# Kernel tuning notes

Hardware: AMD Instinct MI355X
Metric: run time of the kernel (lower is better)

Reference implementation:

```python
import jax, jax.numpy as jnp
import numpy as np
from jax import lax

NUM_CHANNELS = 3
NUM_HEADS = 8
PATCH = 16  # projection_dim = 3 * 16 * 16 = 768
EPS = 1e-5


def setup_inputs() -> dict:
    key = jax.random.key(0)
    ks = jax.random.split(key, 16)
    B, N, D, Hdim = 4, 1024, 768, 3072
    H = NUM_HEADS

    def init(k, shape, fan_in):
        bound = 1.0 / np.sqrt(fan_in)
        return jax.random.uniform(k, shape, jnp.float32, -bound, bound)

    return {
        "x": jax.random.normal(ks[0], (B, N, D), jnp.float32),
        # 3x3 conv QKV projections over per-patch [3,16,16] images (no bias, qkv_bias=False)
        "qconv_w": init(ks[1], (NUM_CHANNELS, NUM_CHANNELS, 3, 3), NUM_CHANNELS * 9),
        "kconv_w": init(ks[2], (NUM_CHANNELS, NUM_CHANNELS, 3, 3), NUM_CHANNELS * 9),
        "vconv_w": init(ks[3], (NUM_CHANNELS, NUM_CHANNELS, 3, 3), NUM_CHANNELS * 9),
        # 1x1 conv mixing heads of the attention map + BatchNorm2d(heads)
        "reatten_w": init(ks[4], (H, H), H),
        "reatten_b": init(ks[5], (H,), H),
        "bn_g": jnp.ones((H,), jnp.float32),
        "bn_b": jnp.zeros((H,), jnp.float32),
        # output projection (Linear dim->dim)
        "proj_w": init(ks[6], (D, D), D),
        "proj_b": init(ks[7], (D,), D),
        # LayerNorm over (num_patches, projection_dim) jointly
        "ln_g": jnp.ones((N, D), jnp.float32),
        "ln_b": jnp.zeros((N, D), jnp.float32),
        # FeedForward
        "ff_w1": init(ks[8], (Hdim, D), D),
        "ff_b1": init(ks[9], (Hdim,), D),
        "ff_w2": init(ks[10], (D, Hdim), Hdim),
        "ff_b2": init(ks[11], (D,), Hdim),
    }


def _conv3x3(x, w):
    # x: [BN, C, p, p], w: [C, C, 3, 3], stride 1, SAME padding
    return lax.conv_general_dilated(x, w, (1, 1), "SAME",
                                    dimension_numbers=("NCHW", "OIHW", "NCHW"))


def _layernorm_2d(x, g, b):
    # LayerNorm over last two axes (N, D) jointly, biased variance, eps=1e-5
    mu = jnp.mean(x, axis=(-2, -1), keepdims=True)
    var = jnp.mean(jnp.square(x - mu), axis=(-2, -1), keepdims=True)
    return (x - mu) * lax.rsqrt(var + EPS) * g + b


def _encoder_fwd(x, qconv_w, kconv_w, vconv_w, reatten_w, reatten_b,
                 bn_g, bn_b, proj_w, proj_b, ln_g, ln_b,
                 ff_w1, ff_b1, ff_w2, ff_b2):
    B, N, D = x.shape
    H = NUM_HEADS
    hd = D // H
    scale = hd ** -0.5

    # --- ReAttention ---
    xi = x.reshape(B * N, NUM_CHANNELS, PATCH, PATCH)

    def qkv(w):
        y = _conv3x3(xi, w).reshape(B, N, H, hd)
        return y.transpose(0, 2, 1, 3)  # [B, H, N, hd]

    q, k, v = qkv(qconv_w), qkv(kconv_w), qkv(vconv_w)

    attn = jax.nn.softmax(jnp.einsum("bhnd,bhmd->bhnm", q, k) * scale, axis=-1)

    # learned cross-head 1x1 conv + BatchNorm2d (training-mode batch stats)
    attn = jnp.einsum("gh,bhnm->bgnm", reatten_w, attn) + reatten_b[None, :, None, None]
    mu = jnp.mean(attn, axis=(0, 2, 3), keepdims=True)
    var = jnp.mean(jnp.square(attn - mu), axis=(0, 2, 3), keepdims=True)
    attn = (attn - mu) * lax.rsqrt(var + EPS)
    attn = attn * bn_g[None, :, None, None] + bn_b[None, :, None, None]

    out = jnp.einsum("bhnm,bhmd->bhnd", attn, v)
    out = out.transpose(0, 2, 1, 3).reshape(B, N, D)
    out = out @ proj_w.T + proj_b

    # --- residual + LN ---
    x1 = _layernorm_2d(x + out, ln_g, ln_b)

    # --- FeedForward (exact GELU) + residual + LN ---
    h = jax.nn.gelu(x1 @ ff_w1.T + ff_b1, approximate=False)
    ff = h @ ff_w2.T + ff_b2
    return _layernorm_2d(x1 + ff, ln_g, ln_b)


def reference(x, qconv_w, kconv_w, vconv_w, reatten_w, reatten_b,
              bn_g, bn_b, proj_w, proj_b, ln_g, ln_b,
              ff_w1, ff_b1, ff_w2, ff_b2):
    return _encoder_fwd(x, qconv_w, kconv_w, vconv_w, reatten_w, reatten_b,
                        bn_g, bn_b, proj_w, proj_b, ln_g, ln_b,
                        ff_w1, ff_b1, ff_w2, ff_b2)
```

## Files before the change

kernel.cpp:

```cpp
#include <hip/hip_runtime.h>
#include <math.h>


typedef unsigned short u16;
typedef unsigned int u32;
typedef __bf16 bf16x8 __attribute__((ext_vector_type(8)));
typedef float f32x4 __attribute__((ext_vector_type(4)));

#define EPSV 1e-5f
#define SL2E 0.14724444620253177f
#define EXPC -11.541560327111707f

__device__ __forceinline__ u16 f2bf(float f) {
  union { float f; u32 u; } v; v.f = f;
  u32 u = v.u + 0x7fffu + ((v.u >> 16) & 1u);
  return (u16)(u >> 16);
}
__device__ __forceinline__ float bf2f(u16 h) {
  union { u32 u; float f; } v; v.u = ((u32)h) << 16; return v.f;
}
__device__ __forceinline__ f32x4 mfma16(bf16x8 a, bf16x8 b, f32x4 c) {
  return __builtin_amdgcn_mfma_f32_16x16x32_bf16(a, b, c, 0, 0, 0);
}
__device__ __forceinline__ void gload16(const void* gp, void* lp) {
  __builtin_amdgcn_global_load_lds(
      (const __attribute__((address_space(1))) u32*)gp,
      (__attribute__((address_space(3))) u32*)lp, 16, 0, 0);
}

struct KS { int off[3]; int hl[3]; };
__device__ __forceinline__ KS ks_init(int t) {
  KS ks;
  int lane = t & 63;
  int lh = lane >> 4, l15 = lane & 15;
  #pragma unroll
  for (int j = 0; j < 3; ++j) {
    int G = j * 512 + t;
    int hl = (G >= 768) ? 1 : 0;
    int C = (G - hl * 768) >> 6;
    int chunk = C / 6, r = C - 6 * chunk;
    int kk = r >> 1, c1 = r & 1;
    int m = chunk * 32 + ((l15 >> 2) << 3) + (c1 << 2) + (l15 & 3);
    ks.off[j] = m * 96 + kk * 32 + lh * 8;
    ks.hl[j] = hl;
  }
  return ks;
}
__device__ __forceinline__ void ks_stage(const u16* __restrict__ khi,
    const u16* __restrict__ klo, size_t rowel, const KS& ks, u16* Kb, int t) {
  int w = t >> 6;
  #pragma unroll
  for (int j = 0; j < 3; ++j) {
    const u16* src = (ks.hl[j] ? klo : khi) + rowel + ks.off[j];
    gload16(src, Kb + (size_t)(j * 512 + w * 64) * 8);
  }
}

__device__ __forceinline__ void qload(const u16* __restrict__ qhi,
    const u16* __restrict__ qlo, size_t qoff, bf16x8* qh, bf16x8* ql) {
  #pragma unroll
  for (int kk = 0; kk < 3; ++kk) {
    qh[kk] = *(const bf16x8*)(qhi + qoff + kk * 32);
    ql[kk] = *(const bf16x8*)(qlo + qoff + kk * 32);
  }
}

__device__ __forceinline__ void score18(const u16* Kb, int mh, int lane,
    const bf16x8* qh, const bf16x8* ql, f32x4& C0, f32x4& C1) {
  C0 = (f32x4){0.f, 0.f, 0.f, 0.f};
  C1 = (f32x4){0.f, 0.f, 0.f, 0.f};
  #pragma unroll
  for (int kk = 0; kk < 3; ++kk) {
    const u16* base = Kb + (mh * 6 + kk * 2) * 512 + lane * 8;
    bf16x8 kh0 = *(const bf16x8*)(base);
    bf16x8 kh1 = *(const bf16x8*)(base + 512);
    bf16x8 kl0 = *(const bf16x8*)(base + 6144);
    bf16x8 kl1 = *(const bf16x8*)(base + 6656);
    C0 = mfma16(kh0, qh[kk], C0);
    C0 = mfma16(kl0, qh[kk], C0);
    C0 = mfma16(kh0, ql[kk], C0);
    C1 = mfma16(kh1, qh[kk], C1);
    C1 = mfma16(kl1, qh[kk], C1);
    C1 = mfma16(kh1, ql[kk], C1);
  }
}

__global__ __launch_bounds__(256) void k_f2b(const float* __restrict__ s,
                                             u16* __restrict__ d, int n) {
  int i = blockIdx.x * 256 + threadIdx.x;
  int stride = gridDim.x * 256;
  for (; i < n; i += stride) d[i] = f2bf(s[i]);
}

__global__ __launch_bounds__(256) void k_conv(const float* __restrict__ x,
    const float* __restrict__ wq, const float* __restrict__ wk, const float* __restrict__ wv,
    u16* __restrict__ qhi, u16* __restrict__ qlo,
    u16* __restrict__ khi, u16* __restrict__ klo,
    float* __restrict__ vb)
{
  __shared__ float patch[768], swq[81], swk[81], swv[81];
  int bid = blockIdx.x;
  int b = bid >> 10, n = bid & 1023;
  int t = threadIdx.x;
  const float* xr = x + (size_t)bid * 768;
  patch[t] = xr[t]; patch[t + 256] = xr[t + 256]; patch[t + 512] = xr[t + 512];
  if (t < 81) { swq[t] = wq[t]; swk[t] = wk[t]; swv[t] = wv[t]; }
  __syncthreads();
  #pragma unroll
  for (int r = 0; r < 3; ++r) {
    int f = t + 256 * r;
    int o = f >> 8, rem = f & 255, pp = rem >> 4, qq = rem & 15;
    float aq = 0.f, ak = 0.f, av = 0.f;
    #pragma unroll
    for (int i = 0; i < 3; ++i)
      #pragma unroll
      for (int dp = 0; dp < 3; ++dp) {
        int ip = pp + dp - 1;
        if (ip < 0 || ip > 15) continue;
        #pragma unroll
        for (int dq = 0; dq < 3; ++dq) {
          int iq = qq + dq - 1;
          if (iq < 0 || iq > 15) continue;
          float pv = patch[i * 256 + ip * 16 + iq];
          int wi = ((o * 3 + i) * 3 + dp) * 3 + dq;
          aq += swq[wi] * pv; ak += swk[wi] * pv; av += swv[wi] * pv;
        }
      }
    int h = f / 96, d = f - h * 96;
    size_t oi = ((size_t)(b * 8 + h) * 1024 + n) * 96 + d;
    float aqs = aq * SL2E;
    u16 qh_ = f2bf(aqs); qhi[oi] = qh_; qlo[oi] = f2bf(aqs - bf2f(qh_));
    u16 kh_ = f2bf(ak);  khi[oi] = kh_; klo[oi] = f2bf(ak - bf2f(kh_));
    vb[oi] = av;
  }
}

__global__ __launch_bounds__(256) void k_vtr(const float* __restrict__ vb,
                                             u16* __restrict__ vtr)
{
  __shared__ u16 lds[12288];
  int bid = blockIdx.x;
  int bh = bid >> 3, n0 = (bid & 7) * 128;
  int t = threadIdx.x;
  int n = t >> 1, dh = (t & 1) * 48;
  const float* src = vb + ((size_t)bh * 1024 + n0 + n) * 96 + dh;
  #pragma unroll
  for (int j4 = 0; j4 < 12; ++j4) {
    float4 v = *(const float4*)(src + j4 * 4);
    int d = dh + j4 * 4;
    lds[(d + 0) * 128 + n] = f2bf(v.x);
    lds[(d + 1) * 128 + n] = f2bf(v.y);
    lds[(d + 2) * 128 + n] = f2bf(v.z);
    lds[(d + 3) * 128 + n] = f2bf(v.w);
  }
  __syncthreads();
  #pragma unroll
  for (int j = 0; j < 48; ++j) {
    int flat = t + 256 * j;
    int d = flat >> 7, n2 = flat & 127;
    vtr[((size_t)bh * 96 + d) * 1024 + n0 + n2] = lds[flat];
  }
}

__global__ __launch_bounds__(512, 4) void k_zpass(
    const u16* __restrict__ qhi, const u16* __restrict__ qlo,
    const u16* __restrict__ khi, const u16* __restrict__ klo,
    float* __restrict__ zp)
{
  __shared__ u16 Kst[2][12288];
  int p = blockIdx.x;
  int s = p >> 3;
  int c = (p & 7) * 4 + (s >> 4);
  int ng = s & 15;
  int b = c >> 3, mg = c & 7;
  int t = threadIdx.x, lane = t & 63, w = t >> 6;
  int l15 = lane & 15, lhi = lane >> 4;
  int nsub = w >> 1, mh = w & 1;
  int n0 = ng * 64 + nsub * 16;
  int m0base = mg * 128;
  KS ks = ks_init(t);
  bf16x8 qh[3], ql[3], qh2[3], ql2[3];
  size_t bh0 = (size_t)(b * 8) * 1024;
  ks_stage(khi, klo, (bh0 + m0base) * 96, ks, Kst[0], t);
  qload(qhi, qlo, (bh0 + n0 + l15) * 96 + lhi * 8, qh, ql);
  __syncthreads();
  #pragma unroll 1
  for (int h = 0; h < 8; ++h) {
    float z = 0.f;
    #pragma unroll
    for (int mt = 0; mt < 2; ++mt) {
      int u = h * 2 + mt;
      if (u < 15) {
        int un = u + 1, hn = un >> 1, mtn = un & 1;
        size_t bhn = (size_t)(b * 8 + hn) * 1024;
        ks_stage(khi, klo, (bhn + m0base + mtn * 64) * 96, ks, Kst[(u + 1) & 1], t);
        if (mtn == 0)
          qload(qhi, qlo, (bhn + n0 + l15) * 96 + lhi * 8, qh2, ql2);
      }
      f32x4 C0, C1;
      score18(Kst[u & 1], mh, lane, qh, ql, C0, C1);
      #pragma unroll
      for (int r = 0; r < 4; ++r)
        z += exp2f(C0[r] + EXPC) + exp2f(C1[r] + EXPC);
      if (u < 15 && mt == 1) {
        #pragma unroll
        for (int kk = 0; kk < 3; ++kk) { qh[kk] = qh2[kk]; ql[kk] = ql2[kk]; }
      }
      __syncthreads();
    }
    z += __shfl_xor(z, 16);
    z += __shfl_xor(z, 32);
    if (lane < 16)
      zp[((size_t)((b * 8 + h) * 16 + mg * 2 + mh)) * 1024 + n0 + lane] = z;
  }
}

__global__ __launch_bounds__(256) void k_zmerge(const float* __restrict__ zp,
                                                float* __restrict__ invZ)
{
  int idx = blockIdx.x * 256 + threadIdx.x;
  int bh = idx >> 10, n = idx & 1023;
  float z = 0.f;
  #pragma unroll
  for (int s = 0; s < 16; ++s) z += zp[((size_t)(bh * 16 + s)) * 1024 + n];
  invZ[idx] = 1.f / z;
}

__global__ __launch_bounds__(512, 2) void k_attn2(
    const u16* __restrict__ qhi, const u16* __restrict__ qlo,
    const u16* __restrict__ khi, const u16* __restrict__ klo,
    const u16* __restrict__ vtr, const float* __restrict__ invZ,
    const float* __restrict__ rw,
    float* __restrict__ U0, float* __restrict__ U1,
    float* __restrict__ U2, float* __restrict__ U3,
    float* __restrict__ pstat)
{
  __shared__ u16 Kst[2][12288];
  __shared__ u16 Plds[32768];
  int p = blockIdx.x;
  int s = p >> 3;
  int c = (p & 7) * 2 + (s >> 4);
  int ng = s & 15;
  int b = c >> 2, mq = c & 3;
  int t = threadIdx.x, lane = t & 63, w = t >> 6;
  int l15 = lane & 15, lhi = lane >> 4;
  int nsub = w >> 1, mh = w & 1;
  int n0 = ng * 64 + nsub * 16;
  int m0q = mq * 256;
  KS ks = ks_init(t);

  float wg[8]; float wsum = 0.f;
  #pragma unroll
  for (int h = 0; h < 8; ++h) { wg[h] = rw[w * 8 + h]; wsum += wg[h]; }
  float cg = -wsum * (1.f / 1024.f);
  f32x4 acc[4][6];
  #pragma unroll
  for (int i = 0; i < 4; ++i)
    #pragma unroll
    for (int ds = 0; ds < 6; ++ds) acc[i][ds] = (f32x4){0.f, 0.f, 0.f, 0.f};
  float sc = 0.f, scc = 0.f;
  size_t vbase = (size_t)(b * 8 + w) * 96;

  bf16x8 qh[3], ql[3], qh2[3], ql2[3];
  size_t bh0 = (size_t)(b * 8) * 1024;
  ks_stage(khi, klo, (bh0 + m0q) * 96, ks, Kst[0], t);
  qload(qhi, qlo, (bh0 + n0 + l15) * 96 + lhi * 8, qh, ql);
  __syncthreads();

  #pragma unroll 1
  for (int mt = 0; mt < 4; ++mt) {
    int m0 = m0q + mt * 64;
    #pragma unroll 1
    for (int h = 0; h < 8; ++h) {
      int u = mt * 8 + h;
      if (u < 31) {
        int hn = (h + 1) & 7;
        int mtn = mt + (h == 7 ? 1 : 0);
        size_t bhn = (size_t)(b * 8 + hn) * 1024;
        ks_stage(khi, klo, (bhn + m0q + mtn * 64) * 96, ks, Kst[(u + 1) & 1], t);
        qload(qhi, qlo, (bhn + n0 + l15) * 96 + lhi * 8, qh2, ql2);
      }
      f32x4 C0, C1;
      score18(Kst[u & 1], mh, lane, qh, ql, C0, C1);
      float iz = invZ[(b * 8 + h) * 1024 + n0 + l15];
      union { u16 us[8]; bf16x8 bv; } pk;
      #pragma unroll
      for (int r = 0; r < 4; ++r) {
        pk.us[r]     = f2bf(exp2f(C0[r] + EXPC) * iz);
        pk.us[4 + r] = f2bf(exp2f(C1[r] + EXPC) * iz);
      }
      *(bf16x8*)&Plds[((h * 8 + w) * 64 + lane) * 8] = pk.bv;
      if (u < 31) {
        #pragma unroll
        for (int kk = 0; kk < 3; ++kk) { qh[kk] = qh2[kk]; ql[kk] = ql2[kk]; }
      }
      if (h < 7) __syncthreads();
    }
    __syncthreads();
    #pragma unroll
    for (int mh2 = 0; mh2 < 2; ++mh2) {
      int mof = m0 + mh2 * 32 + lhi * 8;
      bf16x8 vf[6];
      #pragma unroll
      for (int ds = 0; ds < 6; ++ds)
        vf[ds] = *(const bf16x8*)(vtr + (vbase + ds * 16 + l15) * 1024 + mof);
      #pragma unroll
      for (int ns2 = 0; ns2 < 4; ++ns2) {
        float cm8[8];
        #pragma unroll
        for (int j = 0; j < 8; ++j) cm8[j] = cg;
        #pragma unroll
        for (int h = 0; h < 8; ++h) {
          union { u32 ud[4]; bf16x8 bv; } pf;
          pf.bv = *(const bf16x8*)&Plds[((h * 8 + ns2 * 2 + mh2) * 64 + lane) * 8];
          float wgh = wg[h];
          #pragma unroll
          for (int k2 = 0; k2 < 4; ++k2) {
            union { u32 u; float f; } lo, hi;
            lo.u = pf.ud[k2] << 16;
            hi.u = pf.ud[k2] & 0xffff0000u;
            cm8[2 * k2]     += wgh * lo.f;
            cm8[2 * k2 + 1] += wgh * hi.f;
          }
        }
        union { u16 us[8]; bf16x8 bv; } pk2;
        #pragma unroll
        for (int j = 0; j < 8; ++j) {
          sc += cm8[j]; scc += cm8[j] * cm8[j];
          pk2.us[j] = f2bf(cm8[j]);
        }
        #pragma unroll
        for (int ds = 0; ds < 6; ++ds)
          acc[ns2][ds] = mfma16(pk2.bv, vf[ds], acc[ns2][ds]);
      }
    }
    __syncthreads();
  }

  #pragma unroll
  for (int off = 32; off > 0; off >>= 1) {
    sc += __shfl_down(sc, off); scc += __shfl_down(scc, off);
  }
  if (lane == 0) { pstat[p * 16 + w] = sc; pstat[p * 16 + 8 + w] = scc; }

  float* Uq = (mq == 0) ? U0 : (mq == 1) ? U1 : (mq == 2) ? U2 : U3;
  #pragma unroll
  for (int ns2 = 0; ns2 < 4; ++ns2)
    #pragma unroll
    for (int ds = 0; ds < 6; ++ds)
      #pragma unroll
      for (int r = 0; r < 4; ++r) {
        int n = ng * 64 + ns2 * 16 + lhi * 4 + r;
        Uq[((size_t)(b * 1024 + n)) * 768 + w * 96 + ds * 16 + l15] = acc[ns2][ds][r];
      }
}

__global__ __launch_bounds__(384) void k_vcs(const float* __restrict__ vb,
                                             float* __restrict__ vcs)
{
  __shared__ float part[4][96];
  int bh = blockIdx.x, t = threadIdx.x;
  int c = t % 96, g4 = t / 96;
  float a = 0.f;
  const float* vp = vb + (size_t)bh * 98304 + (size_t)g4 * 24576 + c;
  for (int m = 0; m < 256; ++m) a += vp[m * 96];
  part[g4][c] = a;
  __syncthreads();
  if (t < 96) vcs[bh * 96 + t] = part[0][t] + part[1][t] + part[2][t] + part[3][t];
}

__global__ __launch_bounds__(256) void k_statred(const float* __restrict__ pstat,
                                                 float* __restrict__ stats)
{
  __shared__ float part[16][17];
  int t = threadIdx.x;
  int j = t >> 4, s = t & 15;
  float a = 0.f;
  #pragma unroll
  for (int k2 = 0; k2 < 16; ++k2)
    a += pstat[(size_t)(s + 16 * k2) * 16 + j];
  part[j][s] = a;
  __syncthreads();
  if (t < 16) {
    float v = 0.f;
    #pragma unroll
    for (int s2 = 0; s2 < 16; ++s2) v += part[t][s2];
    stats[t] = v;
  }
}

__global__ __launch_bounds__(256) void k_bnfin(const float* __restrict__ U0,
    const float* __restrict__ U1, const float* __restrict__ U2,
    const float* __restrict__ U3, const float* __restrict__ vcs,
    const float* __restrict__ stats, const float* __restrict__ bng,
    const float* __restrict__ bnb, u16* __restrict__ ubb)
{
  size_t idx = (size_t)blockIdx.x * 256 + threadIdx.x;
  int col = (int)(idx % 768); int i = (int)(idx / 768); int b = i >> 10;
  int g = col / 96, d = col - g * 96;
  const float cnt = 4194304.f;
  float mc = stats[g] / cnt;
  float var = stats[8 + g] / cnt - mc * mc;
  float sg = bng[g] * rsqrtf(var + EPSV);
  float tg = bnb[g] - sg * mc;
  float u = (U0[idx] + U1[idx]) + (U2[idx] + U3[idx]);
  ubb[idx] = f2bf(sg * u + tg * vcs[(b * 8 + g) * 96 + d]);
}

template<int GELU_, int RES_, int STATS_, int BF16OUT>
__global__ __launch_bounds__(256) void k_gemm(
    const u16* __restrict__ A, const u16* __restrict__ W,
    const float* __restrict__ bias, const float* __restrict__ res,
    float* __restrict__ out, u16* __restrict__ outb,
    int K, int Nc, float* __restrict__ stats)
{
  __shared__ u16 As[8192], Bs[8192];
  __shared__ float red[8];
  int t = threadIdx.x, lane = t & 63, wv = t >> 6;
  int l15 = lane & 15, lhi = lane >> 4;
  int i0 = blockIdx.y * 128, j0 = blockIdx.x * 128;
  int wr = wv >> 1, wc = wv & 1;
  f32x4 acc[4][4];
  #pragma unroll
  for (int mi = 0; mi < 4; ++mi)
    #pragma unroll
    for (int ni = 0; ni < 4; ++ni) acc[mi][ni] = (f32x4){0.f, 0.f, 0.f, 0.f};
  int rA = lane >> 3;
  int colel = 8 * ((lane & 7) ^ rA);
  for (int k0 = 0; k0 < K; k0 += 64) {
    if (k0) __syncthreads();
    #pragma unroll
    for (int i = 0; i < 4; ++i) {
      int cA = wv * 4 + i;
      int r = cA * 8 + rA;
      gload16(A + (size_t)(i0 + r) * K + k0 + colel, &As[cA * 512]);
      gload16(W + (size_t)(j0 + r) * K + k0 + colel, &Bs[cA * 512]);
    }
    __syncthreads();
    #pragma unroll
    for (int ks = 0; ks < 2; ++ks) {
      bf16x8 af[4], bf[4];
      #pragma unroll
      for (int mi = 0; mi < 4; ++mi) {
        int r2 = wr * 64 + mi * 16 + l15;
        af[mi] = *(const bf16x8*)&As[r2 * 64 + ((ks * 32 + lhi * 8) ^ (8 * (r2 & 7)))];
      }
      #pragma unroll
      for (int ni = 0; ni < 4; ++ni) {
        int r3 = wc * 64 + ni * 16 + l15;
        bf[ni] = *(const bf16x8*)&Bs[r3 * 64 + ((ks * 32 + lhi * 8) ^ (8 * (r3 & 7)))];
      }
      #pragma unroll
      for (int mi = 0; mi < 4; ++mi)
        #pragma unroll
        for (int ni = 0; ni < 4; ++ni)
          acc[mi][ni] = mfma16(af[mi], bf[ni], acc[mi][ni]);
    }
  }
  float ls = 0.f, lss = 0.f;
  #pragma unroll
  for (int mi = 0; mi < 4; ++mi) {
    #pragma unroll
    for (int ni = 0; ni < 4; ++ni) {
      int col = j0 + wc * 64 + ni * 16 + l15;
      float bv = bias[col];
      #pragma unroll
      for (int r = 0; r < 4; ++r) {
        int row = i0 + wr * 64 + mi * 16 + lhi * 4 + r;
        float val = acc[mi][ni][r] + bv;
        if (RES_) val += res[(size_t)row * Nc + col];
        if (GELU_) val = 0.5f * val * (1.f + erff(val * 0.70710678118654752f));
        if (BF16OUT) outb[(size_t)row * Nc + col] = f2bf(val);
        else out[(size_t)row * Nc + col] = val;
        if (STATS_) { ls += val; lss += val * val; }
      }
    }
  }
  if (STATS_) {
    #pragma unroll
    for (int off = 32; off > 0; off >>= 1) {
      ls += __shfl_down(ls, off); lss += __shfl_down(lss, off);
    }
    if (lane == 0) { red[wv * 2] = ls; red[wv * 2 + 1] = lss; }
    __syncthreads();
    if (t == 0) {
      int b = i0 >> 10;
      atomicAdd(&stats[b * 2],     red[0] + red[2] + red[4] + red[6]);
      atomicAdd(&stats[b * 2 + 1], red[1] + red[3] + red[5] + red[7]);
    }
  }
}

template<int BF16OUT>
__global__ __launch_bounds__(256) void k_ln(const float* __restrict__ y,
    const float* __restrict__ stats, const float* __restrict__ g,
    const float* __restrict__ bta, float* __restrict__ outp, u16* __restrict__ outb)
{
  size_t idx = (size_t)blockIdx.x * 256 + threadIdx.x;
  int i = (int)(idx / 768), col = (int)(idx % 768);
  int b = i >> 10, n = i & 1023;
  const float cnt = 786432.f;
  float mu = stats[b * 2] / cnt;
  float var = stats[b * 2 + 1] / cnt - mu * mu;
  float r = rsqrtf(var + EPSV);
  size_t gi = (size_t)n * 768 + col;
  float v = (y[idx] - mu) * r * g[gi] + bta[gi];
  outp[idx] = v;
  if (BF16OUT) outb[idx] = f2bf(v);
}

extern "C" void kernel_launch(void* const* d_in, const int* in_sizes, int n_in,
                              void* d_out, int out_size, void* d_ws, size_t ws_size,
                              hipStream_t stream)
{
  const float* x   = (const float*)d_in[0];
  const float* qw  = (const float*)d_in[1];
  const float* kw  = (const float*)d_in[2];
  const float* vw  = (const float*)d_in[3];
  const float* rw  = (const float*)d_in[4];
  const float* bng = (const float*)d_in[6];
  const float* bnb = (const float*)d_in[7];
  const float* pw  = (const float*)d_in[8];
  const float* pb  = (const float*)d_in[9];
  const float* lng = (const float*)d_in[10];
  const float* lnb = (const float*)d_in[11];
  const float* fw1 = (const float*)d_in[12];
  const float* fb1 = (const float*)d_in[13];
  const float* fw2 = (const float*)d_in[14];
  const float* fb2 = (const float*)d_in[15];
  float* out = (float*)d_out;

  float* ws    = (float*)d_ws;
  float* stats = ws;
  float* pstat = ws + 64;
  float* vcs   = ws + 4160;
  float* zp    = ws + 7232;
  float* invZ  = ws + 531520;
  float* vb    = ws + 564288;
  float* U0    = ws + 3710016;
  float* U1    = ws + 6855744;
  float* x1    = ws + 10001472;
  u16* u16b = (u16*)(ws + 13147200);
  u16* qhi  = u16b;
  u16* qlo  = u16b + 3145728;
  u16* khi  = u16b + 6291456;
  u16* klo  = u16b + 9437184;
  u16* vtr  = u16b + 12582912;
  u16* ubb  = u16b + 15728640;
  u16* pwb  = u16b + 18874368;
  u16* fw1b = u16b + 19464192;
  u16* fw2b = u16b + 21823488;
  float* U2 = vb;
  float* U3 = x1;
  u16* x1b = qhi;
  u16* hb  = qlo;
  float* y1 = U0;
  float* y2 = vb;

  hipMemsetAsync(stats, 0, 64 * sizeof(float), stream);
  k_f2b<<<1024, 256, 0, stream>>>(pw, pwb, 589824);
  k_f2b<<<2048, 256, 0, stream>>>(fw1, fw1b, 2359296);
  k_f2b<<<2048, 256, 0, stream>>>(fw2, fw2b, 2359296);

  k_conv<<<4096, 256, 0, stream>>>(x, qw, kw, vw, qhi, qlo, khi, klo, vb);
  k_vtr<<<256, 256, 0, stream>>>(vb, vtr);
  k_vcs<<<32, 384, 0, stream>>>(vb, vcs);
  k_zpass<<<512, 512, 0, stream>>>(qhi, qlo, khi, klo, zp);
  k_zmerge<<<128, 256, 0, stream>>>(zp, invZ);
  k_attn2<<<256, 512, 0, stream>>>(qhi, qlo, khi, klo, vtr, invZ, rw,
                                   U0, U1, U2, U3, pstat);
  k_statred<<<1, 256, 0, stream>>>(pstat, stats);
  k_bnfin<<<12288, 256, 0, stream>>>(U0, U1, U2, U3, vcs, stats, bng, bnb, ubb);

  k_gemm<0,1,1,0><<<dim3(6, 32), 256, 0, stream>>>(ubb, pwb, pb, x, y1, nullptr, 768, 768, stats + 16);
  k_ln<1><<<12288, 256, 0, stream>>>(y1, stats + 16, lng, lnb, x1, x1b);
  k_gemm<1,0,0,1><<<dim3(24, 32), 256, 0, stream>>>(x1b, fw1b, fb1, nullptr, nullptr, hb, 768, 3072, nullptr);
  k_gemm<0,1,1,0><<<dim3(6, 32), 256, 0, stream>>>(hb, fw2b, fb2, x1, y2, nullptr, 3072, 768, stats + 24);
  k_ln<0><<<12288, 256, 0, stream>>>(y2, stats + 24, lng, lnb, out, nullptr);
}
```

Before: 339.3 us.

## Materialize unnormalized bf16 scores in zpass and drop score recompute in attention

The first score pass now also writes exp(scores) as bf16 tiles into a 64 MiB workspace buffer. A new mix+PV kernel streams those tiles through double-buffered LDS and folds the head mixing weights and 1/Z into one per-row factor. This removes the second QK^T recompute and collapses the four split-M partial outputs into one U buffer, so bnfin reads a single array. The cost is a large extra HBM write and read of the probability matrix, plus a rearranged workspace layout with aliasing.

```diff
diff --git a/kernel.cpp b/kernel.cpp
--- a/kernel.cpp
+++ b/kernel.cpp
@@ -162,10 +162,10 @@
   }
 }
 
-__global__ __launch_bounds__(512, 4) void k_zpass(
+__global__ __launch_bounds__(512, 2) void k_score(
     const u16* __restrict__ qhi, const u16* __restrict__ qlo,
     const u16* __restrict__ khi, const u16* __restrict__ klo,
-    float* __restrict__ zp)
+    float* __restrict__ zp, u16* __restrict__ pt)
 {
   __shared__ u16 Kst[2][12288];
   int p = blockIdx.x;
@@ -177,6 +177,7 @@
   int l15 = lane & 15, lhi = lane >> 4;
   int nsub = w >> 1, mh = w & 1;
   int n0 = ng * 64 + nsub * 16;
+  int nt = ng * 4 + nsub;
   int m0base = mg * 128;
   KS ks = ks_init(t);
   bf16x8 qh[3], ql[3], qh2[3], ql2[3];
@@ -199,9 +200,17 @@
       }
       f32x4 C0, C1;
       score18(Kst[u & 1], mh, lane, qh, ql, C0, C1);
-      #pragma unroll
-      for (int r = 0; r < 4; ++r)
-        z += exp2f(C0[r] + EXPC) + exp2f(C1[r] + EXPC);
+      union { u16 us[8]; uint4 q4; } pk;
+      #pragma unroll
+      for (int r = 0; r < 4; ++r) {
+        float e0 = exp2f(C0[r] + EXPC);
+        float e1 = exp2f(C1[r] + EXPC);
+        z += e0 + e1;
+        pk.us[r]     = f2bf(e0);
+        pk.us[4 + r] = f2bf(e1);
+      }
+      int mc = mg * 4 + mt * 2 + mh;
+      *(uint4*)&pt[((((size_t)(b * 8 + h) * 32 + mc) * 64 + nt) * 64 + lane) * 8] = pk.q4;
       if (u < 15 && mt == 1) {
         #pragma unroll
         for (int kk = 0; kk < 3; ++kk) { qh[kk] = qh2[kk]; ql[kk] = ql2[kk]; }
@@ -226,114 +235,73 @@
   invZ[idx] = 1.f / z;
 }
 
-__global__ __launch_bounds__(512, 2) void k_attn2(
-    const u16* __restrict__ qhi, const u16* __restrict__ qlo,
-    const u16* __restrict__ khi, const u16* __restrict__ klo,
-    const u16* __restrict__ vtr, const float* __restrict__ invZ,
-    const float* __restrict__ rw,
-    float* __restrict__ U0, float* __restrict__ U1,
-    float* __restrict__ U2, float* __restrict__ U3,
-    float* __restrict__ pstat)
-{
-  __shared__ u16 Kst[2][12288];
-  __shared__ u16 Plds[32768];
+__global__ __launch_bounds__(512, 2) void k_mixpv(
+    const u16* __restrict__ pt, const u16* __restrict__ vtr,
+    const float* __restrict__ invZ, const float* __restrict__ rw,
+    float* __restrict__ U, float* __restrict__ pstat)
+{
+  __shared__ u16 Pst[2][8192];
   int p = blockIdx.x;
-  int s = p >> 3;
-  int c = (p & 7) * 2 + (s >> 4);
-  int ng = s & 15;
-  int b = c >> 2, mq = c & 3;
+  int xcd = p & 7;
+  int b = xcd >> 1, nt = (xcd & 1) * 32 + (p >> 3);
   int t = threadIdx.x, lane = t & 63, w = t >> 6;
   int l15 = lane & 15, lhi = lane >> 4;
-  int nsub = w >> 1, mh = w & 1;
-  int n0 = ng * 64 + nsub * 16;
-  int m0q = mq * 256;
-  KS ks = ks_init(t);
 
   float wg[8]; float wsum = 0.f;
   #pragma unroll
   for (int h = 0; h < 8; ++h) { wg[h] = rw[w * 8 + h]; wsum += wg[h]; }
   float cg = -wsum * (1.f / 1024.f);
-  f32x4 acc[4][6];
-  #pragma unroll
-  for (int i = 0; i < 4; ++i)
-    #pragma unroll
-    for (int ds = 0; ds < 6; ++ds) acc[i][ds] = (f32x4){0.f, 0.f, 0.f, 0.f};
+  float wz[8];
+  #pragma unroll
+  for (int h = 0; h < 8; ++h)
+    wz[h] = wg[h] * invZ[(b * 8 + h) * 1024 + nt * 16 + l15];
+
+  f32x4 acc[6];
+  #pragma unroll
+  for (int ds = 0; ds < 6; ++ds) acc[ds] = (f32x4){0.f, 0.f, 0.f, 0.f};
   float sc = 0.f, scc = 0.f;
   size_t vbase = (size_t)(b * 8 + w) * 96;
-
-  bf16x8 qh[3], ql[3], qh2[3], ql2[3];
-  size_t bh0 = (size_t)(b * 8) * 1024;
-  ks_stage(khi, klo, (bh0 + m0q) * 96, ks, Kst[0], t);
-  qload(qhi, qlo, (bh0 + n0 + l15) * 96 + lhi * 8, qh, ql);
+  size_t pbase = ((size_t)(b * 8 + w) * 32) * 4096 + (size_t)nt * 64;
+
+  gload16(pt + (pbase + lane) * 8, &Pst[0][(size_t)t * 8]);
   __syncthreads();
-
   #pragma unroll 1
-  for (int mt = 0; mt < 4; ++mt) {
-    int m0 = m0q + mt * 64;
-    #pragma unroll 1
+  for (int mc = 0; mc < 32; ++mc) {
+    if (mc < 31)
+      gload16(pt + (pbase + (size_t)(mc + 1) * 4096 + lane) * 8,
+              &Pst[(mc + 1) & 1][(size_t)t * 8]);
+    int mof = mc * 32 + lhi * 8;
+    bf16x8 vf[6];
+    #pragma unroll
+    for (int ds = 0; ds < 6; ++ds)
+      vf[ds] = *(const bf16x8*)(vtr + (vbase + ds * 16 + l15) * 1024 + mof);
+    float cm8[8];
+    #pragma unroll
+    for (int j = 0; j < 8; ++j) cm8[j] = cg;
+    const u16* Pb = &Pst[mc & 1][0];
+    #pragma unroll
     for (int h = 0; h < 8; ++h) {
-      int u = mt * 8 + h;
-      if (u < 31) {
-        int hn = (h + 1) & 7;
-        int mtn = mt + (h == 7 ? 1 : 0);
-        size_t bhn = (size_t)(b * 8 + hn) * 1024;
-        ks_stage(khi, klo, (bhn + m0q + mtn * 64) * 96, ks, Kst[(u + 1) & 1], t);
-        qload(qhi, qlo, (bhn + n0 + l15) * 96 + lhi * 8, qh2, ql2);
-      }
-      f32x4 C0, C1;
-      score18(Kst[u & 1], mh, lane, qh, ql, C0, C1);
-      float iz = invZ[(b * 8 + h) * 1024 + n0 + l15];
-      union { u16 us[8]; bf16x8 bv; } pk;
-      #pragma unroll
-      for (int r = 0; r < 4; ++r) {
-        pk.us[r]     = f2bf(exp2f(C0[r] + EXPC) * iz);
-        pk.us[4 + r] = f2bf(exp2f(C1[r] + EXPC) * iz);
-      }
-      *(bf16x8*)&Plds[((h * 8 + w) * 64 + lane) * 8] = pk.bv;
-      if (u < 31) {
-        #pragma unroll
-        for (int kk = 0; kk < 3; ++kk) { qh[kk] = qh2[kk]; ql[kk] = ql2[kk]; }
-      }
-      if (h < 7) __syncthreads();
-    }
-    __syncthreads();
-    #pragma unroll
-    for (int mh2 = 0; mh2 < 2; ++mh2) {
-      int mof = m0 + mh2 * 32 + lhi * 8;
-      bf16x8 vf[6];
-      #pragma unroll
-      for (int ds = 0; ds < 6; ++ds)
-        vf[ds] = *(const bf16x8*)(vtr + (vbase + ds * 16 + l15) * 1024 + mof);
-      #pragma unroll
-      for (int ns2 = 0; ns2 < 4; ++ns2) {
-        float cm8[8];
-        #pragma unroll
-        for (int j = 0; j < 8; ++j) cm8[j] = cg;
-        #pragma unroll
-        for (int h = 0; h < 8; ++h) {
-          union { u32 ud[4]; bf16x8 bv; } pf;
-          pf.bv = *(const bf16x8*)&Plds[((h * 8 + ns2 * 2 + mh2) * 64 + lane) * 8];
-          float wgh = wg[h];
-          #pragma unroll
-          for (int k2 = 0; k2 < 4; ++k2) {
-            union { u32 u; float f; } lo, hi;
-            lo.u = pf.ud[k2] << 16;
-            hi.u = pf.ud[k2] & 0xffff0000u;
-            cm8[2 * k2]     += wgh * lo.f;
-            cm8[2 * k2 + 1] += wgh * hi.f;
-          }
-        }
-        union { u16 us[8]; bf16x8 bv; } pk2;
-        #pragma unroll
-        for (int j = 0; j < 8; ++j) {
-          sc += cm8[j]; scc += cm8[j] * cm8[j];
-          pk2.us[j] = f2bf(cm8[j]);
-        }
-        #pragma unroll
-        for (int ds = 0; ds < 6; ++ds)
-          acc[ns2][ds] = mfma16(pk2.bv, vf[ds], acc[ns2][ds]);
-      }
-    }
+      union { u32 ud[4]; bf16x8 bv; } pf;
+      pf.bv = *(const bf16x8*)&Pb[(h * 64 + lane) * 8];
+      float wzh = wz[h];
+      #pragma unroll
+      for (int k2 = 0; k2 < 4; ++k2) {
+        union { u32 u; float f; } lo, hi;
+        lo.u = pf.ud[k2] << 16;
+        hi.u = pf.ud[k2] & 0xffff0000u;
+        cm8[2 * k2]     += wzh * lo.f;
+        cm8[2 * k2 + 1] += wzh * hi.f;
+      }
+    }
+    union { u16 us[8]; bf16x8 bv; } pk2;
+    #pragma unroll
+    for (int j = 0; j < 8; ++j) {
+      sc += cm8[j]; scc += cm8[j] * cm8[j];
+      pk2.us[j] = f2bf(cm8[j]);
+    }
+    #pragma unroll
+    for (int ds = 0; ds < 6; ++ds)
+      acc[ds] = mfma16(pk2.bv, vf[ds], acc[ds]);
     __syncthreads();
   }
 
@@ -343,16 +311,13 @@
   }
   if (lane == 0) { pstat[p * 16 + w] = sc; pstat[p * 16 + 8 + w] = scc; }
 
-  float* Uq = (mq == 0) ? U0 : (mq == 1) ? U1 : (mq == 2) ? U2 : U3;
-  #pragma unroll
-  for (int ns2 = 0; ns2 < 4; ++ns2)
-    #pragma unroll
-    for (int ds = 0; ds < 6; ++ds)
-      #pragma unroll
-      for (int r = 0; r < 4; ++r) {
-        int n = ng * 64 + ns2 * 16 + lhi * 4 + r;
-        Uq[((size_t)(b * 1024 + n)) * 768 + w * 96 + ds * 16 + l15] = acc[ns2][ds][r];
-      }
+  #pragma unroll
+  for (int ds = 0; ds < 6; ++ds)
+    #pragma unroll
+    for (int r = 0; r < 4; ++r) {
+      int n = nt * 16 + lhi * 4 + r;
+      U[((size_t)(b * 1024 + n)) * 768 + w * 96 + ds * 16 + l15] = acc[ds][r];
+    }
 }
 
 __global__ __launch_bounds__(384) void k_vcs(const float* __restrict__ vb,
@@ -389,11 +354,10 @@
   }
 }
 
-__global__ __launch_bounds__(256) void k_bnfin(const float* __restrict__ U0,
-    const float* __restrict__ U1, const float* __restrict__ U2,
-    const float* __restrict__ U3, const float* __restrict__ vcs,
-    const float* __restrict__ stats, const float* __restrict__ bng,
-    const float* __restrict__ bnb, u16* __restrict__ ubb)
+__global__ __launch_bounds__(256) void k_bnfin(const float* __restrict__ U,
+    const float* __restrict__ vcs, const float* __restrict__ stats,
+    const float* __restrict__ bng, const float* __restrict__ bnb,
+    u16* __restrict__ ubb)
 {
   size_t idx = (size_t)blockIdx.x * 256 + threadIdx.x;
   int col = (int)(idx % 768); int i = (int)(idx / 768); int b = i >> 10;
@@ -403,8 +367,7 @@
   float var = stats[8 + g] / cnt - mc * mc;
   float sg = bng[g] * rsqrtf(var + EPSV);
   float tg = bnb[g] - sg * mc;
-  float u = (U0[idx] + U1[idx]) + (U2[idx] + U3[idx]);
-  ubb[idx] = f2bf(sg * u + tg * vcs[(b * 8 + g) * 96 + d]);
+  ubb[idx] = f2bf(sg * U[idx] + tg * vcs[(b * 8 + g) * 96 + d]);
 }
 
 template<int GELU_, int RES_, int STATS_, int BF16OUT>
@@ -530,32 +493,29 @@
   const float* fb2 = (const float*)d_in[15];
   float* out = (float*)d_out;
 
-  float* ws    = (float*)d_ws;
-  float* stats = ws;
-  float* pstat = ws + 64;
-  float* vcs   = ws + 4160;
-  float* zp    = ws + 7232;
-  float* invZ  = ws + 531520;
-  float* vb    = ws + 564288;
-  float* U0    = ws + 3710016;
-  float* U1    = ws + 6855744;
-  float* x1    = ws + 10001472;
-  u16* u16b = (u16*)(ws + 13147200);
-  u16* qhi  = u16b;
-  u16* qlo  = u16b + 3145728;
-  u16* khi  = u16b + 6291456;
-  u16* klo  = u16b + 9437184;
-  u16* vtr  = u16b + 12582912;
-  u16* ubb  = u16b + 15728640;
-  u16* pwb  = u16b + 18874368;
-  u16* fw1b = u16b + 19464192;
-  u16* fw2b = u16b + 21823488;
-  float* U2 = vb;
-  float* U3 = x1;
-  u16* x1b = qhi;
-  u16* hb  = qlo;
+  u16* pt   = (u16*)d_ws;
+  float* vb = (float*)pt;
+  u16* hb   = pt;
+  float* y2 = (float*)pt + 12582912;
+  float* fsm = (float*)(pt + 33554432);
+  float* stats = fsm;
+  float* pstat = fsm + 64;
+  float* vcs   = fsm + 4160;
+  float* zp    = fsm + 7232;
+  float* invZ  = fsm + 531520;
+  u16* qhi  = (u16*)(fsm + 564288);
+  u16* qlo  = qhi + 3145728;
+  u16* khi  = qlo + 3145728;
+  u16* klo  = khi + 3145728;
+  u16* vtrb = klo + 3145728;
+  u16* pwb  = vtrb + 3145728;
+  u16* fw1b = pwb + 589824;
+  u16* fw2b = fw1b + 2359296;
+  float* U0 = (float*)qhi;
+  float* x1 = (float*)khi;
   float* y1 = U0;
-  float* y2 = vb;
+  u16* ubb  = vtrb;
+  u16* x1b  = vtrb;
 
   hipMemsetAsync(stats, 0, 64 * sizeof(float), stream);
   k_f2b<<<1024, 256, 0, stream>>>(pw, pwb, 589824);
@@ -563,14 +523,13 @@
   k_f2b<<<2048, 256, 0, stream>>>(fw2, fw2b, 2359296);
 
   k_conv<<<4096, 256, 0, stream>>>(x, qw, kw, vw, qhi, qlo, khi, klo, vb);
-  k_vtr<<<256, 256, 0, stream>>>(vb, vtr);
+  k_vtr<<<256, 256, 0, stream>>>(vb, vtrb);
   k_vcs<<<32, 384, 0, stream>>>(vb, vcs);
-  k_zpass<<<512, 512, 0, stream>>>(qhi, qlo, khi, klo, zp);
+  k_score<<<512, 512, 0, stream>>>(qhi, qlo, khi, klo, zp, pt);
   k_zmerge<<<128, 256, 0, stream>>>(zp, invZ);
-  k_attn2<<<256, 512, 0, stream>>>(qhi, qlo, khi, klo, vtr, invZ, rw,
-                                   U0, U1, U2, U3, pstat);
+  k_mixpv<<<256, 512, 0, stream>>>(pt, vtrb, invZ, rw, U0, pstat);
   k_statred<<<1, 256, 0, stream>>>(pstat, stats);
-  k_bnfin<<<12288, 256, 0, stream>>>(U0, U1, U2, U3, vcs, stats, bng, bnb, ubb);
+  k_bnfin<<<12288, 256, 0, stream>>>(U0, vcs, stats, bng, bnb, ubb);
 
   k_gemm<0,1,1,0><<<dim3(6, 32), 256, 0, stream>>>(ubb, pwb, pb, x, y1, nullptr, 768, 768, stats + 16);
   k_ln<1><<<12288, 256, 0, stream>>>(y1, stats + 16, lng, lnb, x1, x1b);
```

Measured after the change: 299.5 us. -11.7%, faster.
